# Kernel optimization log

Measured on AMD Instinct MI355X. Metric: run time of the kernel, lower is better.

Reference implementation:

```python
import jax, jax.numpy as jnp
import numpy as np


def setup_inputs() -> dict:
    key = jax.random.key(0)
    B, D, C, H = 4096, 64, 128, 512
    ks = jax.random.split(key, 6)
    return {
        "q_z_x_params": jax.random.normal(ks[0], (B, C), jnp.float32),
        "eps": jax.random.normal(ks[1], (B, D), jnp.float32),
        "W1": jax.random.normal(ks[2], (D + C, H), jnp.float32) / np.sqrt(D + C).astype(np.float32),
        "b1": jnp.zeros((H,), jnp.float32),
        "W2": jax.random.normal(ks[3], (H, H), jnp.float32) / np.sqrt(H).astype(np.float32),
        "b2": jnp.zeros((H,), jnp.float32),
        "W3": jax.random.normal(ks[4], (H, 2 * D), jnp.float32) / np.sqrt(H).astype(np.float32),
        "b3": jnp.zeros((2 * D,), jnp.float32),
    }


def _made_masks(D, C, H):
    # Standard MADE degrees, natural ordering; context columns fully connected.
    m_in = np.arange(1, D + 1)                      # input degrees 1..D
    m_h = (np.arange(H) % (D - 1)) + 1              # hidden degrees 1..D-1
    M1 = np.concatenate([m_h[None, :] >= m_in[:, None],
                         np.ones((C, H), bool)], axis=0)   # (D+C, H)
    M2 = m_h[None, :] >= m_h[:, None]               # (H, H)
    m_out = np.tile(np.arange(1, D + 1), 2)         # (2D,) mean||prescale
    M3 = m_out[None, :] > m_h[:, None]              # (H, 2D)
    f32 = jnp.float32
    return jnp.asarray(M1, f32), jnp.asarray(M2, f32), jnp.asarray(M3, f32)


def reference(q_z_x_params, eps, W1, b1, W2, b2, W3, b3):
    B, D = eps.shape
    C = q_z_x_params.shape[1]
    H = W2.shape[0]
    M1, M2, M3 = _made_masks(D, C, H)
    mW1, mW2, mW3 = W1 * M1, W2 * M2, W3 * M3

    def made(z):
        x = jnp.concatenate([z, q_z_x_params], axis=1)   # (B, D+C)
        h1 = jax.nn.relu(x @ mW1 + b1)
        h2 = jax.nn.relu(h1 @ mW2 + b2)
        out = h2 @ mW3 + b3                              # (B, 2D)
        return out[:, :D], out[:, D:]

    def step(z, i):
        mean, prescale = made(z)
        mu_i = jnp.take(mean, i, axis=1)                 # (B,)
        scale_i = jax.nn.softplus(jnp.take(prescale, i, axis=1))
        z_i = mu_i + scale_i * jnp.take(eps, i, axis=1)  # reparameterized Normal sample
        z = z.at[:, i].set(z_i)
        return z, None

    z0 = jnp.zeros((B, D), eps.dtype)
    z_sample, _ = jax.lax.scan(step, z0, jnp.arange(D))
    return z_sample
```

## Files before the change

kernel.cpp:

```cpp
#include <hip/hip_runtime.h>
#include <math.h>

#define DD 64
#define CC 128
#define HH 512
#define BATCH 4096

typedef __attribute__((ext_vector_type(2))) float f32x2;
typedef unsigned long long u64;

__device__ __forceinline__ f32x2 splat2(float x) { f32x2 v; v[0] = x; v[1] = x; return v; }
__device__ __forceinline__ f32x2 lo2(float4 v) { f32x2 r; r[0] = v.x; r[1] = v.y; return r; }
__device__ __forceinline__ f32x2 hi2(float4 v) { f32x2 r; r[0] = v.z; r[1] = v.w; return r; }

__device__ __forceinline__ f32x2 pk_fma_s(u64 hpair, f32x2 b, f32x2 c) {
    f32x2 d;
    asm("v_pk_fma_f32 %0, %1, %2, %3" : "=v"(d) : "s"(hpair), "v"(b), "v"(c));
    return d;
}

__device__ __forceinline__ float fast_softplus(float x) {
    float t = exp2f(-fabsf(x) * 1.44269504f);
    return fmaxf(x, 0.f) + 0.69314718f * log2f(1.f + t);
}

__device__ __forceinline__ float bcast(float x, int l) {
    return __int_as_float(__builtin_amdgcn_readlane(__float_as_int(x), l));
}
__device__ __forceinline__ u64 rl_pair(float x, int l) {
    unsigned u = (unsigned)__builtin_amdgcn_readlane(__float_as_int(x), l);
    return ((u64)u << 32) | u;
}

typedef const __attribute__((address_space(1))) void* as1_cptr;
typedef __attribute__((address_space(3))) void* as3_ptr;
typedef const __attribute__((address_space(3))) float* as3c;
__device__ __forceinline__ void glds16(const float* g, float* l) {
    __builtin_amdgcn_global_load_lds((as1_cptr)g, (as3_ptr)l, 16, 0, 0);
}

__device__ __forceinline__ float4 ldsb128(const float* p) {
    float4 r;
    asm volatile("ds_read_b128 %0, %1" : "=v"(r) : "v"((as3c)p));
    return r;
}
__device__ __forceinline__ f32x2 ldsr2(const float* p) {
    f32x2 r;
    asm volatile("ds_read2_b32 %0, %1 offset0:0 offset1:64" : "=v"(r) : "v"((as3c)p));
    return r;
}

__global__ __launch_bounds__(256, 2) void made_sample(
    const float* __restrict__ ctx,
    const float* __restrict__ eps,
    const float* __restrict__ W1,
    const float* __restrict__ b1,
    const float* __restrict__ W2,
    const float* __restrict__ b2,
    const float* __restrict__ W3,
    const float* __restrict__ b3,
    float* __restrict__ out)
{
    const int lane  = threadIdx.x & 63;
    const int w     = threadIdx.x >> 6;
    const int rbase = blockIdx.x * 8 + w * 2;
    const int jbase = 8 * lane;

    __shared__ float sbuf[2][10 * HH];
    __shared__ float w3sb[2][5 * 256];

    int deg[8];
    #pragma unroll
    for (int u = 0; u < 8; ++u) deg[u] = (jbase + u) % 63 + 1;

    auto stage_row = [&](const float* src, float* dst) {
        glds16(src + lane * 8,     dst);
        glds16(src + lane * 8 + 4, dst + 256);
    };
    auto stage_w3pair = [&](int k0, int k1, float* dst) {
        const float* g = (lane < 32) ? (W3 + k0 * (2 * DD) + lane * 4)
                                     : (W3 + k1 * (2 * DD) + (lane - 32) * 4);
        glds16(g, dst);
    };

    f32x2 p1[2][4], p2[2][4];
    #pragma unroll
    for (int j = 0; j < 4; ++j) {
        f32x2 t1, t2;
        t1[0] = b1[jbase + 2 * j]; t1[1] = b1[jbase + 2 * j + 1];
        t2[0] = b2[jbase + 2 * j]; t2[1] = b2[jbase + 2 * j + 1];
        p1[0][j] = t1; p1[1][j] = t1;
        p2[0][j] = t2; p2[1][j] = t2;
    }
    f32x2 accA[2], accB[2];
    accA[0] = splat2(0.f); accA[1] = splat2(0.f);
    accB[0] = splat2(0.f); accB[1] = splat2(0.f);

    float ca[2], cb[2], ep[2];
    #pragma unroll
    for (int r = 0; r < 2; ++r) {
        ca[r] = ctx[(rbase + r) * CC + lane];
        cb[r] = ctx[(rbase + r) * CC + 64 + lane];
        ep[r] = eps[(rbase + r) * DD + lane];
    }
    const float b3m = b3[lane];
    const float b3p = b3[64 + lane];

    auto stage_ctx = [&](int ch, float* buf) {
        stage_row(W1 + (DD + 8 * ch + 2 * w) * HH,     buf + (2 * w) * HH);
        stage_row(W1 + (DD + 8 * ch + 2 * w + 1) * HH, buf + (2 * w + 1) * HH);
    };
    auto stage_step = [&](int in, float* buf, float* w3buf) {
        if (in == 0) {
            if (w == 1) stage_row(W1, buf + 9 * HH);
            return;
        }
        const int basen = in - 1;
        const bool h9n = basen < 8;
        stage_row(W2 + (basen + 63 * w) * HH,       buf + w * HH);
        stage_row(W2 + (basen + 63 * (4 + w)) * HH, buf + (4 + w) * HH);
        if (w == 0 && h9n) stage_row(W2 + (basen + 504) * HH, buf + 8 * HH);
        if (w == 1) stage_row(W1 + in * HH, buf + 9 * HH);
        stage_w3pair(basen + 63 * (2 * w), basen + 63 * (2 * w + 1),
                     w3buf + w * 256);
        if (w == 2 && h9n)
            stage_w3pair(basen + 504, basen + 504, w3buf + 4 * 256);
    };

    stage_ctx(0, sbuf[0]);
    __syncthreads();
    #pragma unroll 1
    for (int ch = 0; ch < 16; ++ch) {
        float* cur = sbuf[ch & 1];
        if (ch < 15) stage_ctx(ch + 1, sbuf[(ch + 1) & 1]);
        else         stage_step(0, sbuf[0], w3sb[0]);
        const float* lb = cur + lane * 4;
        float4 cwL[8], cwH[8];
        #pragma unroll
        for (int q = 0; q < 8; ++q) {
            cwL[q] = ldsb128(lb + q * HH);
            cwH[q] = ldsb128(lb + q * HH + 256);
        }
        asm volatile("s_waitcnt lgkmcnt(0)" ::: "memory");
        __builtin_amdgcn_sched_barrier(0);
        #pragma unroll
        for (int q = 0; q < 8; ++q) {
            const int c = 8 * ch + q;
            #pragma unroll
            for (int r = 0; r < 2; ++r) {
                const u64 cvp = rl_pair((ch < 8) ? ca[r] : cb[r], c & 63);
                p1[r][0] = pk_fma_s(cvp, lo2(cwL[q]), p1[r][0]);
                p1[r][1] = pk_fma_s(cvp, hi2(cwL[q]), p1[r][1]);
                p1[r][2] = pk_fma_s(cvp, lo2(cwH[q]), p1[r][2]);
                p1[r][3] = pk_fma_s(cvp, hi2(cwH[q]), p1[r][3]);
            }
        }
        __syncthreads();
    }

    float z[2] = {0.f, 0.f};

    #pragma unroll 1
    for (int i = 0; i < DD; ++i) {
        float* cur = sbuf[i & 1];
        const float* w3s = w3sb[i & 1];

        if (i < 63) stage_step(i + 1, sbuf[(i + 1) & 1], w3sb[(i + 1) & 1]);

        const float* lb = cur + lane * 4;
        float4 wL[9], wH[9];
        f32x2 w3v[9];
        if (i > 0) {
            #pragma unroll
            for (int t = 0; t < 9; ++t) {
                wL[t] = ldsb128(lb + t * HH);
                wH[t] = ldsb128(lb + t * HH + 256);
            }
            #pragma unroll
            for (int t = 0; t < 9; ++t) w3v[t] = ldsr2(w3s + t * 128 + lane);
        }
        const float4 w1L = ldsb128(lb + 9 * HH);
        const float4 w1H = ldsb128(lb + 9 * HH + 256);
        asm volatile("s_waitcnt lgkmcnt(0)" ::: "memory");
        __builtin_amdgcn_sched_barrier(0);

        if (i > 0) {
            const int base = i - 1;
            const bool h9 = base < 8;

            float m[2];
            #pragma unroll
            for (int r = 0; r < 2; ++r) {
                float s[8];
                #pragma unroll
                for (int u = 0; u < 8; ++u)
                    s[u] = (deg[u] == i) ? p1[r][u >> 1][u & 1] : 0.f;
                const float sv = ((s[0] + s[1]) + (s[2] + s[3]))
                               + ((s[4] + s[5]) + (s[6] + s[7]));
                m[r] = fmaxf(sv, 0.f);
            }

            #pragma unroll
            for (int t = 0; t < 8; ++t) {
                const int k = base + 63 * t;
                const u64 h0 = rl_pair(m[0], k >> 3);
                const u64 h1 = rl_pair(m[1], k >> 3);
                p2[0][0] = pk_fma_s(h0, lo2(wL[t]), p2[0][0]);
                p2[0][1] = pk_fma_s(h0, hi2(wL[t]), p2[0][1]);
                p2[0][2] = pk_fma_s(h0, lo2(wH[t]), p2[0][2]);
                p2[0][3] = pk_fma_s(h0, hi2(wH[t]), p2[0][3]);
                p2[1][0] = pk_fma_s(h1, lo2(wL[t]), p2[1][0]);
                p2[1][1] = pk_fma_s(h1, hi2(wL[t]), p2[1][1]);
                p2[1][2] = pk_fma_s(h1, lo2(wH[t]), p2[1][2]);
                p2[1][3] = pk_fma_s(h1, hi2(wH[t]), p2[1][3]);
            }
            if (h9) {
                const u64 h0 = rl_pair(m[0], 63);
                const u64 h1 = rl_pair(m[1], 63);
                p2[0][0] = pk_fma_s(h0, lo2(wL[8]), p2[0][0]);
                p2[0][1] = pk_fma_s(h0, hi2(wL[8]), p2[0][1]);
                p2[0][2] = pk_fma_s(h0, lo2(wH[8]), p2[0][2]);
                p2[0][3] = pk_fma_s(h0, hi2(wH[8]), p2[0][3]);
                p2[1][0] = pk_fma_s(h1, lo2(wL[8]), p2[1][0]);
                p2[1][1] = pk_fma_s(h1, hi2(wL[8]), p2[1][1]);
                p2[1][2] = pk_fma_s(h1, lo2(wH[8]), p2[1][2]);
                p2[1][3] = pk_fma_s(h1, hi2(wH[8]), p2[1][3]);
            }

            float g[2];
            #pragma unroll
            for (int r = 0; r < 2; ++r) {
                float s[8];
                #pragma unroll
                for (int u = 0; u < 8; ++u)
                    s[u] = (deg[u] == i) ? p2[r][u >> 1][u & 1] : 0.f;
                const float sv = ((s[0] + s[1]) + (s[2] + s[3]))
                               + ((s[4] + s[5]) + (s[6] + s[7]));
                g[r] = fmaxf(sv, 0.f);
            }

            #pragma unroll
            for (int t = 0; t < 8; ++t) {
                const int k = base + 63 * t;
                const u64 h0 = rl_pair(g[0], k >> 3);
                const u64 h1 = rl_pair(g[1], k >> 3);
                if (t & 1) {
                    accB[0] = pk_fma_s(h0, w3v[t], accB[0]);
                    accB[1] = pk_fma_s(h1, w3v[t], accB[1]);
                } else {
                    accA[0] = pk_fma_s(h0, w3v[t], accA[0]);
                    accA[1] = pk_fma_s(h1, w3v[t], accA[1]);
                }
            }
            if (h9) {
                const u64 h0 = rl_pair(g[0], 63);
                const u64 h1 = rl_pair(g[1], 63);
                accB[0] = pk_fma_s(h0, w3v[8], accB[0]);
                accB[1] = pk_fma_s(h1, w3v[8], accB[1]);
            }
        }

        {
            #pragma unroll
            for (int r = 0; r < 2; ++r) {
                const f32x2 at = accA[r] + accB[r];
                const float am = at[0] + b3m;
                const float ap = at[1] + b3p;
                const float sp = fast_softplus(ap);
                const float zc = fmaf(sp, ep[r], am);
                const float zi = bcast(zc, i);
                if (lane == i) z[r] = zi;
                const u64 zp = rl_pair(zc, i);
                p1[r][0] = pk_fma_s(zp, lo2(w1L), p1[r][0]);
                p1[r][1] = pk_fma_s(zp, hi2(w1L), p1[r][1]);
                p1[r][2] = pk_fma_s(zp, lo2(w1H), p1[r][2]);
                p1[r][3] = pk_fma_s(zp, hi2(w1H), p1[r][3]);
            }
        }

        __syncthreads();
    }

    #pragma unroll
    for (int r = 0; r < 2; ++r) out[(rbase + r) * DD + lane] = z[r];
}

extern "C" void kernel_launch(void* const* d_in, const int* in_sizes, int n_in,
                              void* d_out, int out_size, void* d_ws, size_t ws_size,
                              hipStream_t stream) {
    const float* ctx = (const float*)d_in[0];
    const float* eps = (const float*)d_in[1];
    const float* W1  = (const float*)d_in[2];
    const float* b1  = (const float*)d_in[3];
    const float* W2  = (const float*)d_in[4];
    const float* b2  = (const float*)d_in[5];
    const float* W3  = (const float*)d_in[6];
    const float* b3  = (const float*)d_in[7];
    (void)d_ws; (void)ws_size; (void)in_sizes; (void)n_in; (void)out_size;

    made_sample<<<BATCH / 8, 256, 0, stream>>>(ctx, eps, W1, b1, W2, b2, W3, b3,
                                               (float*)d_out);
}
```

Before: 189.5 us.

## Triple-buffer LDS weight staging with vmcnt waits and a single barrier per step

Moves from double to triple buffering of the LDS weight staging, issuing loads two steps ahead. The full __syncthreads is replaced by per-wave s_waitcnt vmcnt counts plus one s_barrier. Stage_step now always issues the same number of loads, clamping the row index, so the vmcnt counts stay fixed. The asm ds_read batches are replaced by plain LDS loads placed next to their FMAs, giving the compiler room to schedule. The cost is about 50% more shared memory, which can limit the 2 blocks per CU occupancy, extra redundant loads for the clamped row, and hand-counted vmcnt values that must match the issued loads exactly.

Result: faster. 185.2 us (-2.3%).

```diff
diff --git a/kernel.cpp b/kernel.cpp
--- a/kernel.cpp
+++ b/kernel.cpp
@@ -10,8 +10,6 @@
 typedef unsigned long long u64;
 
 __device__ __forceinline__ f32x2 splat2(float x) { f32x2 v; v[0] = x; v[1] = x; return v; }
-__device__ __forceinline__ f32x2 lo2(float4 v) { f32x2 r; r[0] = v.x; r[1] = v.y; return r; }
-__device__ __forceinline__ f32x2 hi2(float4 v) { f32x2 r; r[0] = v.z; r[1] = v.w; return r; }
 
 __device__ __forceinline__ f32x2 pk_fma_s(u64 hpair, f32x2 b, f32x2 c) {
     f32x2 d;
@@ -34,21 +32,12 @@
 
 typedef const __attribute__((address_space(1))) void* as1_cptr;
 typedef __attribute__((address_space(3))) void* as3_ptr;
-typedef const __attribute__((address_space(3))) float* as3c;
 __device__ __forceinline__ void glds16(const float* g, float* l) {
     __builtin_amdgcn_global_load_lds((as1_cptr)g, (as3_ptr)l, 16, 0, 0);
 }
 
-__device__ __forceinline__ float4 ldsb128(const float* p) {
-    float4 r;
-    asm volatile("ds_read_b128 %0, %1" : "=v"(r) : "v"((as3c)p));
-    return r;
-}
-__device__ __forceinline__ f32x2 ldsr2(const float* p) {
-    f32x2 r;
-    asm volatile("ds_read2_b32 %0, %1 offset0:0 offset1:64" : "=v"(r) : "v"((as3c)p));
-    return r;
-}
+#define WAIT_VM(N) asm volatile("s_waitcnt vmcnt(" #N ")" ::: "memory")
+#define CFENCE()   asm volatile("" ::: "memory")
 
 __global__ __launch_bounds__(256, 2) void made_sample(
     const float* __restrict__ ctx,
@@ -66,13 +55,19 @@
     const int rbase = blockIdx.x * 8 + w * 2;
     const int jbase = 8 * lane;
 
-    __shared__ float sbuf[2][10 * HH];
-    __shared__ float w3sb[2][5 * 256];
+    __shared__ float sbuf[3][10 * HH];
+    __shared__ float w3sb[3][5 * 256];
 
     int deg[8];
     #pragma unroll
     for (int u = 0; u < 8; ++u) deg[u] = (jbase + u) % 63 + 1;
 
+    auto load8v = [&](const float* base_, f32x2* r_) {
+        float4 a = *(const float4*)(base_ + lane * 4);
+        float4 b = *(const float4*)(base_ + 256 + lane * 4);
+        r_[0][0] = a.x; r_[0][1] = a.y; r_[1][0] = a.z; r_[1][1] = a.w;
+        r_[2][0] = b.x; r_[2][1] = b.y; r_[3][0] = b.z; r_[3][1] = b.w;
+    };
     auto stage_row = [&](const float* src, float* dst) {
         glds16(src + lane * 8,     dst);
         glds16(src + lane * 8 + 4, dst + 256);
@@ -111,78 +106,66 @@
         stage_row(W1 + (DD + 8 * ch + 2 * w + 1) * HH, buf + (2 * w + 1) * HH);
     };
     auto stage_step = [&](int in, float* buf, float* w3buf) {
-        if (in == 0) {
-            if (w == 1) stage_row(W1, buf + 9 * HH);
-            return;
-        }
-        const int basen = in - 1;
-        const bool h9n = basen < 8;
+        const int basen = (in == 0) ? 0 : (in - 1);
+        const int r8 = (basen + 504 < HH) ? (basen + 504) : (HH - 1);
         stage_row(W2 + (basen + 63 * w) * HH,       buf + w * HH);
         stage_row(W2 + (basen + 63 * (4 + w)) * HH, buf + (4 + w) * HH);
-        if (w == 0 && h9n) stage_row(W2 + (basen + 504) * HH, buf + 8 * HH);
+        if (w == 0) stage_row(W2 + r8 * HH, buf + 8 * HH);
         if (w == 1) stage_row(W1 + in * HH, buf + 9 * HH);
         stage_w3pair(basen + 63 * (2 * w), basen + 63 * (2 * w + 1),
                      w3buf + w * 256);
-        if (w == 2 && h9n)
-            stage_w3pair(basen + 504, basen + 504, w3buf + 4 * 256);
+        if (w == 2) stage_w3pair(r8, r8, w3buf + 4 * 256);
+    };
+    auto wait_step = [&]() {
+        if (w == 0 || w == 1) WAIT_VM(7);
+        else if (w == 2)      WAIT_VM(6);
+        else                  WAIT_VM(5);
     };
 
     stage_ctx(0, sbuf[0]);
-    __syncthreads();
+    stage_ctx(1, sbuf[1]);
+    int bc = 0;
     #pragma unroll 1
     for (int ch = 0; ch < 16; ++ch) {
-        float* cur = sbuf[ch & 1];
-        if (ch < 15) stage_ctx(ch + 1, sbuf[(ch + 1) & 1]);
-        else         stage_step(0, sbuf[0], w3sb[0]);
-        const float* lb = cur + lane * 4;
-        float4 cwL[8], cwH[8];
+        if (ch < 15) WAIT_VM(4); else WAIT_VM(0);
+        __builtin_amdgcn_s_barrier();
+        CFENCE();
+        __builtin_amdgcn_sched_barrier(0);
+        const int b2i = (bc < 1) ? bc + 2 : bc - 1;
+        if (ch < 14) stage_ctx(ch + 2, sbuf[b2i]);
+        float* cur = sbuf[bc];
         #pragma unroll
         for (int q = 0; q < 8; ++q) {
-            cwL[q] = ldsb128(lb + q * HH);
-            cwH[q] = ldsb128(lb + q * HH + 256);
+            f32x2 cw[4];
+            load8v(cur + q * HH, cw);
+            const int c = 8 * ch + q;
+            #pragma unroll
+            for (int r = 0; r < 2; ++r) {
+                const u64 cvp = rl_pair((ch < 8) ? ca[r] : cb[r], c & 63);
+                #pragma unroll
+                for (int j = 0; j < 4; ++j) p1[r][j] = pk_fma_s(cvp, cw[j], p1[r][j]);
+            }
         }
-        asm volatile("s_waitcnt lgkmcnt(0)" ::: "memory");
-        __builtin_amdgcn_sched_barrier(0);
-        #pragma unroll
-        for (int q = 0; q < 8; ++q) {
-            const int c = 8 * ch + q;
-            #pragma unroll
-            for (int r = 0; r < 2; ++r) {
-                const u64 cvp = rl_pair((ch < 8) ? ca[r] : cb[r], c & 63);
-                p1[r][0] = pk_fma_s(cvp, lo2(cwL[q]), p1[r][0]);
-                p1[r][1] = pk_fma_s(cvp, hi2(cwL[q]), p1[r][1]);
-                p1[r][2] = pk_fma_s(cvp, lo2(cwH[q]), p1[r][2]);
-                p1[r][3] = pk_fma_s(cvp, hi2(cwH[q]), p1[r][3]);
-            }
-        }
-        __syncthreads();
-    }
+        bc = (bc < 2) ? bc + 1 : 0;
+    }
+    __syncthreads();
 
     float z[2] = {0.f, 0.f};
+    stage_step(0, sbuf[0], w3sb[0]);
+    stage_step(1, sbuf[1], w3sb[1]);
+    bc = 0;
 
     #pragma unroll 1
     for (int i = 0; i < DD; ++i) {
-        float* cur = sbuf[i & 1];
-        const float* w3s = w3sb[i & 1];
-
-        if (i < 63) stage_step(i + 1, sbuf[(i + 1) & 1], w3sb[(i + 1) & 1]);
-
-        const float* lb = cur + lane * 4;
-        float4 wL[9], wH[9];
-        f32x2 w3v[9];
-        if (i > 0) {
-            #pragma unroll
-            for (int t = 0; t < 9; ++t) {
-                wL[t] = ldsb128(lb + t * HH);
-                wH[t] = ldsb128(lb + t * HH + 256);
-            }
-            #pragma unroll
-            for (int t = 0; t < 9; ++t) w3v[t] = ldsr2(w3s + t * 128 + lane);
-        }
-        const float4 w1L = ldsb128(lb + 9 * HH);
-        const float4 w1H = ldsb128(lb + 9 * HH + 256);
-        asm volatile("s_waitcnt lgkmcnt(0)" ::: "memory");
+        if (i < 63) wait_step(); else WAIT_VM(0);
+        __builtin_amdgcn_s_barrier();
+        CFENCE();
         __builtin_amdgcn_sched_barrier(0);
+
+        float* cur = sbuf[bc];
+        const float* w3s = w3sb[bc];
+        const int b2i = (bc < 1) ? bc + 2 : bc - 1;
+        if (i < 62) stage_step(i + 2, sbuf[b2i], w3sb[b2i]);
 
         if (i > 0) {
             const int base = i - 1;
@@ -203,28 +186,26 @@
             #pragma unroll
             for (int t = 0; t < 8; ++t) {
                 const int k = base + 63 * t;
+                f32x2 wv[4];
+                load8v(cur + t * HH, wv);
                 const u64 h0 = rl_pair(m[0], k >> 3);
                 const u64 h1 = rl_pair(m[1], k >> 3);
-                p2[0][0] = pk_fma_s(h0, lo2(wL[t]), p2[0][0]);
-                p2[0][1] = pk_fma_s(h0, hi2(wL[t]), p2[0][1]);
-                p2[0][2] = pk_fma_s(h0, lo2(wH[t]), p2[0][2]);
-                p2[0][3] = pk_fma_s(h0, hi2(wH[t]), p2[0][3]);
-                p2[1][0] = pk_fma_s(h1, lo2(wL[t]), p2[1][0]);
-                p2[1][1] = pk_fma_s(h1, hi2(wL[t]), p2[1][1]);
-                p2[1][2] = pk_fma_s(h1, lo2(wH[t]), p2[1][2]);
-                p2[1][3] = pk_fma_s(h1, hi2(wH[t]), p2[1][3]);
+                #pragma unroll
+                for (int j = 0; j < 4; ++j) {
+                    p2[0][j] = pk_fma_s(h0, wv[j], p2[0][j]);
+                    p2[1][j] = pk_fma_s(h1, wv[j], p2[1][j]);
+                }
             }
             if (h9) {
+                f32x2 wv[4];
+                load8v(cur + 8 * HH, wv);
                 const u64 h0 = rl_pair(m[0], 63);
                 const u64 h1 = rl_pair(m[1], 63);
-                p2[0][0] = pk_fma_s(h0, lo2(wL[8]), p2[0][0]);
-                p2[0][1] = pk_fma_s(h0, hi2(wL[8]), p2[0][1]);
-                p2[0][2] = pk_fma_s(h0, lo2(wH[8]), p2[0][2]);
-                p2[0][3] = pk_fma_s(h0, hi2(wH[8]), p2[0][3]);
-                p2[1][0] = pk_fma_s(h1, lo2(wL[8]), p2[1][0]);
-                p2[1][1] = pk_fma_s(h1, hi2(wL[8]), p2[1][1]);
-                p2[1][2] = pk_fma_s(h1, lo2(wH[8]), p2[1][2]);
-                p2[1][3] = pk_fma_s(h1, hi2(wH[8]), p2[1][3]);
+                #pragma unroll
+                for (int j = 0; j < 4; ++j) {
+                    p2[0][j] = pk_fma_s(h0, wv[j], p2[0][j]);
+                    p2[1][j] = pk_fma_s(h1, wv[j], p2[1][j]);
+                }
             }
 
             float g[2];
@@ -242,25 +223,33 @@
             #pragma unroll
             for (int t = 0; t < 8; ++t) {
                 const int k = base + 63 * t;
+                f32x2 w3v;
+                w3v[0] = w3s[t * 128 + lane];
+                w3v[1] = w3s[t * 128 + 64 + lane];
                 const u64 h0 = rl_pair(g[0], k >> 3);
                 const u64 h1 = rl_pair(g[1], k >> 3);
                 if (t & 1) {
-                    accB[0] = pk_fma_s(h0, w3v[t], accB[0]);
-                    accB[1] = pk_fma_s(h1, w3v[t], accB[1]);
+                    accB[0] = pk_fma_s(h0, w3v, accB[0]);
+                    accB[1] = pk_fma_s(h1, w3v, accB[1]);
                 } else {
-                    accA[0] = pk_fma_s(h0, w3v[t], accA[0]);
-                    accA[1] = pk_fma_s(h1, w3v[t], accA[1]);
+                    accA[0] = pk_fma_s(h0, w3v, accA[0]);
+                    accA[1] = pk_fma_s(h1, w3v, accA[1]);
                 }
             }
             if (h9) {
+                f32x2 w3v;
+                w3v[0] = w3s[8 * 128 + lane];
+                w3v[1] = w3s[8 * 128 + 64 + lane];
                 const u64 h0 = rl_pair(g[0], 63);
                 const u64 h1 = rl_pair(g[1], 63);
-                accB[0] = pk_fma_s(h0, w3v[8], accB[0]);
-                accB[1] = pk_fma_s(h1, w3v[8], accB[1]);
+                accB[0] = pk_fma_s(h0, w3v, accB[0]);
+                accB[1] = pk_fma_s(h1, w3v, accB[1]);
             }
         }
 
         {
+            f32x2 w1v[4];
+            load8v(cur + 9 * HH, w1v);
             #pragma unroll
             for (int r = 0; r < 2; ++r) {
                 const f32x2 at = accA[r] + accB[r];
@@ -271,14 +260,12 @@
                 const float zi = bcast(zc, i);
                 if (lane == i) z[r] = zi;
                 const u64 zp = rl_pair(zc, i);
-                p1[r][0] = pk_fma_s(zp, lo2(w1L), p1[r][0]);
-                p1[r][1] = pk_fma_s(zp, hi2(w1L), p1[r][1]);
-                p1[r][2] = pk_fma_s(zp, lo2(w1H), p1[r][2]);
-                p1[r][3] = pk_fma_s(zp, hi2(w1H), p1[r][3]);
+                #pragma unroll
+                for (int j = 0; j < 4; ++j) p1[r][j] = pk_fma_s(zp, w1v[j], p1[r][j]);
             }
         }
 
-        __syncthreads();
+        bc = (bc < 2) ? bc + 1 : 0;
     }
 
     #pragma unroll
```
